# Optimization experiments

Hardware: AMD Instinct MI355X
Metric: run time of the kernel (lower is better)

## Reference

```python
import jax, jax.numpy as jnp
import numpy as np

B, N, C = 8, 1024, 768
H = 12
HD = C // H
R = 16  # LoRA rank
SCALE = HD ** -0.5


def setup_inputs() -> dict:
    key = jax.random.key(0)
    ks = jax.random.split(key, 13)
    s = C ** -0.5
    return {
        "x": jax.random.normal(ks[0], (B, N, C), jnp.float32),
        "Wq": jax.random.normal(ks[1], (C, C), jnp.float32) * s,
        "Wk": jax.random.normal(ks[2], (C, C), jnp.float32) * s,
        "Wv": jax.random.normal(ks[3], (C, C), jnp.float32) * s,
        "Wp": jax.random.normal(ks[4], (C, C), jnp.float32) * s,
        "bp": jax.random.normal(ks[5], (C,), jnp.float32) * 0.02,
        "la_q": jax.random.normal(ks[6], (C, R), jnp.float32) * s,
        "lb_q": jax.random.normal(ks[7], (R, C), jnp.float32) * (R ** -0.5),
        "la_k": jax.random.normal(ks[8], (C, R), jnp.float32) * s,
        "lb_k": jax.random.normal(ks[9], (R, C), jnp.float32) * (R ** -0.5),
        "la_v": jax.random.normal(ks[10], (C, R), jnp.float32) * s,
        "lb_v": jax.random.normal(ks[11], (R, C), jnp.float32) * (R ** -0.5),
        "block_weight": jax.random.uniform(ks[12], (3,), jnp.float32),
    }


def _split_heads(t):
    # [B, N, C] -> [B, H, N, HD]
    return t.reshape(B, N, H, HD).transpose(0, 2, 1, 3)


def reference(x, Wq, Wk, Wv, Wp, bp, la_q, lb_q, la_k, lb_k, la_v, lb_v, block_weight):
    # q/k/v projections (qkv_bias=False) + LoRA adapter injection (msa=[1,1,1])
    q = x @ Wq + block_weight[0] * ((x @ la_q) @ lb_q)
    k = x @ Wk + block_weight[1] * ((x @ la_k) @ lb_k)
    v = x @ Wv + block_weight[2] * ((x @ la_v) @ lb_v)

    qh = _split_heads(q)  # [B,H,N,HD]
    kh = _split_heads(k)
    vh = _split_heads(v)

    # full NxN scores, scale, softmax (attn_drop=0 -> identity)
    attn = jnp.einsum("bhnd,bhmd->bhnm", qh, kh) * SCALE
    attn = jax.nn.softmax(attn, axis=-1)
    out = jnp.einsum("bhnm,bhmd->bhnd", attn, vh)  # [B,H,N,HD]
    out = out.transpose(0, 2, 1, 3).reshape(B, N, C)

    # output projection (proj_drop=0 -> identity)
    return out @ Wp + bp
```

## Files before the change

kernel.cpp:

```cpp
#include <hip/hip_runtime.h>

#define BB 8
#define NN 1024
#define CC 768
#define HH 12
#define HD 64
#define RR 16
#define MM (BB * NN)
#define WSZ (CC * CC)

#define KSC 0.18033688011112042f

typedef short bf16x8 __attribute__((ext_vector_type(8)));
typedef short bf16x4 __attribute__((ext_vector_type(4)));
typedef float f32x4 __attribute__((ext_vector_type(4)));

__device__ __forceinline__ unsigned short f2bf(float f) {
    unsigned u = __builtin_bit_cast(unsigned, f);
    unsigned r = (u + 0x7FFFu + ((u >> 16) & 1u)) >> 16;
    return (unsigned short)r;
}
__device__ __forceinline__ float bf2f(unsigned short s) {
    return __builtin_bit_cast(float, ((unsigned)s) << 16);
}

__global__ __launch_bounds__(256) void prep_w(
    const float* __restrict__ Wq, const float* __restrict__ Wk,
    const float* __restrict__ Wv, const float* __restrict__ Wp,
    const float* __restrict__ la_q, const float* __restrict__ lb_q,
    const float* __restrict__ la_k, const float* __restrict__ lb_k,
    const float* __restrict__ la_v, const float* __restrict__ lb_v,
    const float* __restrict__ bw, short* __restrict__ wt_hi,
    short* __restrict__ wt_lo) {
    __shared__ float laS[64][16];
    __shared__ float lbS[16][64];
    __shared__ float T[64][65];

    const int z = blockIdx.z;
    const int k0 = blockIdx.y * 64, n0 = blockIdx.x * 64;
    const int tid = threadIdx.x;

    const float* W = (z == 0) ? Wq : (z == 1) ? Wk : (z == 2) ? Wv : Wp;
    const float* la = (z == 0) ? la_q : (z == 1) ? la_k : la_v;
    const float* lb = (z == 0) ? lb_q : (z == 1) ? lb_k : lb_v;
    const float bwz = (z < 3) ? bw[z] : 0.f;

    if (z < 3) {
        #pragma unroll
        for (int e = 0; e < 4; ++e) {
            int idx = tid + 256 * e;
            laS[idx >> 4][idx & 15] = la[(size_t)(k0 + (idx >> 4)) * RR + (idx & 15)];
            lbS[idx >> 6][idx & 63] = lb[(size_t)(idx >> 6) * CC + n0 + (idx & 63)];
        }
    }
    __syncthreads();

    #pragma unroll
    for (int e = 0; e < 16; ++e) {
        int idx = tid + 256 * e;
        int row = idx >> 6, col = idx & 63;
        float v = W[(size_t)(k0 + row) * CC + n0 + col];
        if (z < 3) {
            float s = 0.f;
            #pragma unroll
            for (int r = 0; r < 16; ++r) s += laS[row][r] * lbS[r][col];
            v += bwz * s;
        }
        T[row][col] = v;
    }
    __syncthreads();

    short* oh = wt_hi + (size_t)z * WSZ;
    short* ol = wt_lo + (size_t)z * WSZ;
    #pragma unroll
    for (int e = 0; e < 16; ++e) {
        int idx = tid + 256 * e;
        int nrow = idx >> 6, kcol = idx & 63;
        float v = T[kcol][nrow];
        unsigned short hi = f2bf(v);
        unsigned short lo = f2bf(v - bf2f(hi));
        size_t off = (size_t)(n0 + nrow) * CC + k0 + kcol;
        oh[off] = (short)hi;
        ol[off] = (short)lo;
    }
}

__global__ __launch_bounds__(256) void prep_cvt(const float* __restrict__ src,
                                                short* __restrict__ hi,
                                                short* __restrict__ lo, int n4) {
    int i = blockIdx.x * 256 + threadIdx.x;
    const int stride = gridDim.x * 256;
    for (; i < n4; i += stride) {
        f32x4 v = ((const f32x4*)src)[i];
        bf16x4 h, l;
        #pragma unroll
        for (int c = 0; c < 4; ++c) {
            unsigned short hh = f2bf(v[c]);
            h[c] = (short)hh;
            l[c] = (short)f2bf(v[c] - bf2f(hh));
        }
        ((bf16x4*)hi)[i] = h;
        ((bf16x4*)lo)[i] = l;
    }
}

#define LW 40

__device__ __forceinline__ void gemm_core(
    const short* __restrict__ gAh, const short* __restrict__ gAl, int rowA0,
    const short* __restrict__ gBh, const short* __restrict__ gBl, int rowB0,
    short* AsH, short* AsL, short* BsH, short* BsL, f32x4 acc[4][4]) {
    const int tid = threadIdx.x;
    const int lane = tid & 63;
    const int w = tid >> 6;
    const int wm = w >> 1, wn = w & 1;
    const int p = lane & 15, g = lane >> 4;

    const int srow = tid >> 2;
    const int scc = (tid & 3) * 8;

    for (int kt = 0; kt < CC; kt += 32) {
        #pragma unroll
        for (int q = 0; q < 2; ++q) {
            int row = srow + 64 * q;
            size_t ga = (size_t)(rowA0 + row) * CC + kt + scc;
            size_t gb = (size_t)(rowB0 + row) * CC + kt + scc;
            bf16x8 ah = *(const bf16x8*)(gAh + ga);
            bf16x8 al = *(const bf16x8*)(gAl + ga);
            bf16x8 bh = *(const bf16x8*)(gBh + gb);
            bf16x8 bl = *(const bf16x8*)(gBl + gb);
            *(bf16x8*)(AsH + row * LW + scc) = ah;
            *(bf16x8*)(AsL + row * LW + scc) = al;
            *(bf16x8*)(BsH + row * LW + scc) = bh;
            *(bf16x8*)(BsL + row * LW + scc) = bl;
        }
        __syncthreads();

        bf16x8 a_h[4], a_l[4], b_h[4], b_l[4];
        #pragma unroll
        for (int i = 0; i < 4; ++i) {
            int arow = wm * 64 + i * 16 + p;
            int brow = wn * 64 + i * 16 + p;
            a_h[i] = *(const bf16x8*)(AsH + arow * LW + g * 8);
            a_l[i] = *(const bf16x8*)(AsL + arow * LW + g * 8);
            b_h[i] = *(const bf16x8*)(BsH + brow * LW + g * 8);
            b_l[i] = *(const bf16x8*)(BsL + brow * LW + g * 8);
        }
        #pragma unroll
        for (int i = 0; i < 4; ++i) {
            #pragma unroll
            for (int j = 0; j < 4; ++j) {
                acc[i][j] = __builtin_amdgcn_mfma_f32_16x16x32_bf16(
                    a_h[i], b_h[j], acc[i][j], 0, 0, 0);
                acc[i][j] = __builtin_amdgcn_mfma_f32_16x16x32_bf16(
                    a_h[i], b_l[j], acc[i][j], 0, 0, 0);
                acc[i][j] = __builtin_amdgcn_mfma_f32_16x16x32_bf16(
                    a_l[i], b_h[j], acc[i][j], 0, 0, 0);
            }
        }
        __syncthreads();
    }
}

__global__ __launch_bounds__(256, 2) void gemm_qkv(
    const short* __restrict__ xh, const short* __restrict__ xl,
    const short* __restrict__ wth, const short* __restrict__ wtl,
    short* __restrict__ qb, short* __restrict__ kb, short* __restrict__ vtb) {
    __shared__ __align__(16) short AsH[128 * LW], AsL[128 * LW];
    __shared__ __align__(16) short BsH[128 * LW], BsL[128 * LW];

    const int z = blockIdx.z;
    const int m0 = blockIdx.y * 128, c0 = blockIdx.x * 128;
    const short* wzh = wth + (size_t)z * WSZ;
    const short* wzl = wtl + (size_t)z * WSZ;

    f32x4 acc[4][4];
    const f32x4 z4 = {0.f, 0.f, 0.f, 0.f};
    #pragma unroll
    for (int i = 0; i < 4; ++i)
        #pragma unroll
        for (int j = 0; j < 4; ++j) acc[i][j] = z4;

    const int lane = threadIdx.x & 63, w = threadIdx.x >> 6;
    const int wm = w >> 1, wn = w & 1, p = lane & 15, g = lane >> 4;

    if (z < 2) {
        gemm_core(xh, xl, m0, wzh, wzl, c0, AsH, AsL, BsH, BsL, acc);
        short* dst = (z == 0) ? qb : kb;
        #pragma unroll
        for (int i = 0; i < 4; ++i) {
            #pragma unroll
            for (int r = 0; r < 4; ++r) {
                int m = m0 + wm * 64 + i * 16 + 4 * g + r;
                int b = m >> 10, n = m & 1023;
                #pragma unroll
                for (int j = 0; j < 4; ++j) {
                    int c = c0 + wn * 64 + j * 16 + p;
                    int h = c >> 6, d = c & 63;
                    dst[(((size_t)(b * HH + h)) * NN + n) * HD + d] =
                        (short)f2bf(acc[i][j][r]);
                }
            }
        }
    } else {
        gemm_core(wzh, wzl, c0, xh, xl, m0, AsH, AsL, BsH, BsL, acc);
        #pragma unroll
        for (int i = 0; i < 4; ++i) {
            #pragma unroll
            for (int r = 0; r < 4; ++r) {
                int c = c0 + wm * 64 + i * 16 + 4 * g + r;
                int h = c >> 6, d = c & 63;
                #pragma unroll
                for (int j = 0; j < 4; ++j) {
                    int m = m0 + wn * 64 + j * 16 + p;
                    int b = m >> 10, n = m & 1023;
                    vtb[(((size_t)(b * HH + h)) * HD + d) * NN + n] =
                        (short)f2bf(acc[i][j][r]);
                }
            }
        }
    }
}

#define AW 72

__global__ __launch_bounds__(256) void attn(const short* __restrict__ qb,
                                            const short* __restrict__ kb,
                                            const short* __restrict__ vtb,
                                            short* __restrict__ aoh,
                                            short* __restrict__ aol) {
    __shared__ __align__(16) short Qs[64 * AW], Ks[64 * AW], Vts[64 * AW];
    __shared__ __align__(16) short Ps[4][16 * AW];

    const int bh = blockIdx.y, q0 = blockIdx.x * 64;
    const int tid = threadIdx.x, lane = tid & 63, w = tid >> 6;
    const int p = lane & 15, g = lane >> 4;
    const short* qp = qb + (size_t)bh * NN * HD;
    const short* kp = kb + (size_t)bh * NN * HD;
    const short* vp = vtb + (size_t)bh * NN * HD;

    #pragma unroll
    for (int e = 0; e < 2; ++e) {
        int idx = tid + 256 * e;
        int row = idx >> 3, c8 = (idx & 7) * 8;
        *(bf16x8*)(Qs + row * AW + c8) =
            *(const bf16x8*)(qp + (size_t)(q0 + row) * HD + c8);
    }
    __syncthreads();
    bf16x8 bQ[2];
    #pragma unroll
    for (int ks = 0; ks < 2; ++ks)
        bQ[ks] = *(const bf16x8*)(Qs + (w * 16 + p) * AW + g * 8 + 32 * ks);

    float m_run = -1e30f, l_run = 0.f;
    f32x4 oacc[4];
    const f32x4 z4 = {0.f, 0.f, 0.f, 0.f};
    #pragma unroll
    for (int df = 0; df < 4; ++df) oacc[df] = z4;
    short* Pw = &Ps[w][0];

    for (int t = 0; t < NN / 64; ++t) {
        if (t) __syncthreads();
        const int j0 = t * 64;
        #pragma unroll
        for (int e = 0; e < 2; ++e) {
            int idx = tid + 256 * e;
            int row = idx >> 3, c8 = (idx & 7) * 8;
            *(bf16x8*)(Ks + row * AW + c8) =
                *(const bf16x8*)(kp + (size_t)(j0 + row) * HD + c8);
            *(bf16x8*)(Vts + row * AW + c8) =
                *(const bf16x8*)(vp + (size_t)row * NN + j0 + c8);
        }
        __syncthreads();

        f32x4 sacc[4];
        #pragma unroll
        for (int jf = 0; jf < 4; ++jf) sacc[jf] = z4;
        #pragma unroll
        for (int ks = 0; ks < 2; ++ks) {
            #pragma unroll
            for (int jf = 0; jf < 4; ++jf) {
                bf16x8 aK =
                    *(const bf16x8*)(Ks + (jf * 16 + p) * AW + g * 8 + 32 * ks);
                sacc[jf] = __builtin_amdgcn_mfma_f32_16x16x32_bf16(
                    aK, bQ[ks], sacc[jf], 0, 0, 0);
            }
        }

        float tmax = -1e30f;
        #pragma unroll
        for (int jf = 0; jf < 4; ++jf)
            #pragma unroll
            for (int r = 0; r < 4; ++r) tmax = fmaxf(tmax, sacc[jf][r]);
        tmax = fmaxf(tmax, __shfl_xor(tmax, 16));
        tmax = fmaxf(tmax, __shfl_xor(tmax, 32));
        const float mnew = fmaxf(m_run, tmax);
        const float fac = exp2f((m_run - mnew) * KSC);
        m_run = mnew;
        float lsum = 0.f;
        bf16x4 pk[4];
        #pragma unroll
        for (int jf = 0; jf < 4; ++jf) {
            #pragma unroll
            for (int r = 0; r < 4; ++r) {
                float e = exp2f((sacc[jf][r] - mnew) * KSC);
                lsum += e;
                pk[jf][r] = (short)f2bf(e);
            }
        }
        lsum += __shfl_xor(lsum, 16);
        lsum += __shfl_xor(lsum, 32);
        l_run = l_run * fac + lsum;

        #pragma unroll
        for (int jf = 0; jf < 4; ++jf)
            *(bf16x4*)(Pw + p * AW + jf * 16 + 4 * g) = pk[jf];
        asm volatile("s_waitcnt lgkmcnt(0)" ::: "memory");
        __builtin_amdgcn_sched_barrier(0);

        #pragma unroll
        for (int r = 0; r < 4; ++r) {
            float fr = __shfl(fac, 4 * g + r, 16);
            #pragma unroll
            for (int df = 0; df < 4; ++df) oacc[df][r] *= fr;
        }

        #pragma unroll
        for (int ks = 0; ks < 2; ++ks) {
            bf16x8 aP = *(const bf16x8*)(Pw + p * AW + g * 8 + 32 * ks);
            #pragma unroll
            for (int df = 0; df < 4; ++df) {
                bf16x8 bV =
                    *(const bf16x8*)(Vts + (df * 16 + p) * AW + g * 8 + 32 * ks);
                oacc[df] = __builtin_amdgcn_mfma_f32_16x16x32_bf16(
                    aP, bV, oacc[df], 0, 0, 0);
            }
        }
    }

    const float inv = 1.f / l_run;
    const int b = bh / HH, h = bh % HH;
    #pragma unroll
    for (int r = 0; r < 4; ++r) {
        float ir = __shfl(inv, 4 * g + r, 16);
        int n = q0 + w * 16 + 4 * g + r;
        #pragma unroll
        for (int df = 0; df < 4; ++df) {
            float v = oacc[df][r] * ir;
            unsigned short hi = f2bf(v);
            unsigned short lo = f2bf(v - bf2f(hi));
            size_t off = ((size_t)(b * NN + n)) * CC + h * HD + df * 16 + p;
            aoh[off] = (short)hi;
            aol[off] = (short)lo;
        }
    }
}

__global__ __launch_bounds__(256, 2) void gemm_proj(
    const short* __restrict__ aoh, const short* __restrict__ aol,
    const short* __restrict__ wth, const short* __restrict__ wtl,
    const float* __restrict__ bp, float* __restrict__ out) {
    __shared__ __align__(16) short AsH[128 * LW], AsL[128 * LW];
    __shared__ __align__(16) short BsH[128 * LW], BsL[128 * LW];

    const int m0 = blockIdx.y * 128, c0 = blockIdx.x * 128;
    const short* wph = wth + (size_t)3 * WSZ;
    const short* wpl = wtl + (size_t)3 * WSZ;

    f32x4 acc[4][4];
    const f32x4 z4 = {0.f, 0.f, 0.f, 0.f};
    #pragma unroll
    for (int i = 0; i < 4; ++i)
        #pragma unroll
        for (int j = 0; j < 4; ++j) acc[i][j] = z4;

    gemm_core(aoh, aol, m0, wph, wpl, c0, AsH, AsL, BsH, BsL, acc);

    const int lane = threadIdx.x & 63, w = threadIdx.x >> 6;
    const int wm = w >> 1, wn = w & 1, p = lane & 15, g = lane >> 4;

    float bpv[4];
    #pragma unroll
    for (int j = 0; j < 4; ++j) bpv[j] = bp[c0 + wn * 64 + j * 16 + p];

    #pragma unroll
    for (int i = 0; i < 4; ++i) {
        #pragma unroll
        for (int r = 0; r < 4; ++r) {
            int m = m0 + wm * 64 + i * 16 + 4 * g + r;
            #pragma unroll
            for (int j = 0; j < 4; ++j) {
                int c = c0 + wn * 64 + j * 16 + p;
                out[(size_t)m * CC + c] = acc[i][j][r] + bpv[j];
            }
        }
    }
}

extern "C" void kernel_launch(void* const* d_in, const int* in_sizes, int n_in,
                              void* d_out, int out_size, void* d_ws,
                              size_t ws_size, hipStream_t stream) {
    const float* x = (const float*)d_in[0];
    const float* Wq = (const float*)d_in[1];
    const float* Wk = (const float*)d_in[2];
    const float* Wv = (const float*)d_in[3];
    const float* Wp = (const float*)d_in[4];
    const float* bp = (const float*)d_in[5];
    const float* la_q = (const float*)d_in[6];
    const float* lb_q = (const float*)d_in[7];
    const float* la_k = (const float*)d_in[8];
    const float* lb_k = (const float*)d_in[9];
    const float* la_v = (const float*)d_in[10];
    const float* lb_v = (const float*)d_in[11];
    const float* bw = (const float*)d_in[12];
    float* out = (float*)d_out;

    short* ws = (short*)d_ws;
    short* wt_hi = ws;
    short* wt_lo = wt_hi + (size_t)4 * WSZ;
    short* x_hi = wt_lo + (size_t)4 * WSZ;
    short* x_lo = x_hi + (size_t)MM * CC;
    short* qbuf = x_lo + (size_t)MM * CC;
    short* kbuf = qbuf + (size_t)MM * CC;
    short* vtbuf = kbuf + (size_t)MM * CC;
    short* aoh = vtbuf + (size_t)MM * CC;
    short* aol = aoh + (size_t)MM * CC;

    prep_w<<<dim3(CC / 64, CC / 64, 4), 256, 0, stream>>>(
        Wq, Wk, Wv, Wp, la_q, lb_q, la_k, lb_k, la_v, lb_v, bw, wt_hi, wt_lo);
    prep_cvt<<<2048, 256, 0, stream>>>(x, x_hi, x_lo, MM * CC / 4);
    gemm_qkv<<<dim3(CC / 128, MM / 128, 3), 256, 0, stream>>>(
        x_hi, x_lo, wt_hi, wt_lo, qbuf, kbuf, vtbuf);
    attn<<<dim3(NN / 64, BB * HH), 256, 0, stream>>>(qbuf, kbuf, vtbuf, aoh, aol);
    gemm_proj<<<dim3(CC / 128, MM / 128), 256, 0, stream>>>(aoh, aol, wt_hi,
                                                            wt_lo, bp, out);
}
```

Baseline: 331.4 us.

## Double-buffer GEMM and attention tiles with direct global-to-LDS loads and XCD swizzle

Replaces register-staged global loads with global_load_lds into MFMA-fragment-ordered LDS layouts, double-buffered so the next K tile (GEMMs) or K/V tile (attention) loads while the current one computes. Adds block-index swizzling so neighbouring tiles land on the same XCD for L2 reuse. Attention also skips the rescale of the output accumulator when no row max changes, using a wave-wide __any check. LDS use grows (64KB per GEMM block), which may limit occupancy, and correctness relies on the async LDS writes being complete at each barrier.

```diff
diff --git a/kernel.cpp b/kernel.cpp
--- a/kernel.cpp
+++ b/kernel.cpp
@@ -8,6 +8,7 @@
 #define RR 16
 #define MM (BB * NN)
 #define WSZ (CC * CC)
+#define NT (NN / 64)
 
 #define KSC 0.18033688011112042f
 
@@ -22,6 +23,12 @@
 }
 __device__ __forceinline__ float bf2f(unsigned short s) {
     return __builtin_bit_cast(float, ((unsigned)s) << 16);
+}
+
+__device__ __forceinline__ void gload16(const void* g, void* l) {
+    __builtin_amdgcn_global_load_lds(
+        (const __attribute__((address_space(1))) unsigned int*)g,
+        (__attribute__((address_space(3))) unsigned int*)l, 16, 0, 0);
 }
 
 __global__ __launch_bounds__(256) void prep_w(
@@ -104,60 +111,76 @@
     }
 }
 
-#define LW 40
-
-__device__ __forceinline__ void gemm_core(
-    const short* __restrict__ gAh, const short* __restrict__ gAl, int rowA0,
-    const short* __restrict__ gBh, const short* __restrict__ gBl, int rowB0,
-    short* AsH, short* AsL, short* BsH, short* BsL, f32x4 acc[4][4]) {
-    const int tid = threadIdx.x;
-    const int lane = tid & 63;
-    const int w = tid >> 6;
+__device__ __forceinline__ void stage_gemm(const short* __restrict__ gAh,
+                                           const short* __restrict__ gAl,
+                                           const short* __restrict__ gBh,
+                                           const short* __restrict__ gBl,
+                                           int rowA0, int rowB0, int kt,
+                                           short* Lb, int tid) {
+    const int fr = ((tid >> 6) << 4) | (tid & 15);
+    const int kc = ((tid >> 4) & 3) * 8 + kt;
+    const size_t ga0 = (size_t)(rowA0 + fr) * CC + kc;
+    const size_t ga1 = ga0 + (size_t)64 * CC;
+    const size_t gb0 = (size_t)(rowB0 + fr) * CC + kc;
+    const size_t gb1 = gb0 + (size_t)64 * CC;
+    short* d0 = Lb + tid * 8;
+    short* d1 = Lb + (tid + 256) * 8;
+    gload16(gAh + ga0, d0);
+    gload16(gAh + ga1, d1);
+    gload16(gAl + ga0, d0 + 4096);
+    gload16(gAl + ga1, d1 + 4096);
+    gload16(gBh + gb0, d0 + 8192);
+    gload16(gBh + gb1, d1 + 8192);
+    gload16(gBl + gb0, d0 + 12288);
+    gload16(gBl + gb1, d1 + 12288);
+}
+
+__device__ __forceinline__ void gemm_compute(const short* Lb, int wm, int wn,
+                                             int lane, f32x4 acc[4][4]) {
+    const int fb = lane * 8;
+    const short* AH = Lb;
+    const short* AL = Lb + 4096;
+    const short* BH = Lb + 8192;
+    const short* BL = Lb + 12288;
+    bf16x8 ah[4], al[4], bh[4], bl[4];
+    #pragma unroll
+    for (int i = 0; i < 4; ++i) {
+        ah[i] = *(const bf16x8*)(AH + (wm * 4 + i) * 512 + fb);
+        al[i] = *(const bf16x8*)(AL + (wm * 4 + i) * 512 + fb);
+    }
+    #pragma unroll
+    for (int j = 0; j < 4; ++j) {
+        bh[j] = *(const bf16x8*)(BH + (wn * 4 + j) * 512 + fb);
+        bl[j] = *(const bf16x8*)(BL + (wn * 4 + j) * 512 + fb);
+    }
+    #pragma unroll
+    for (int i = 0; i < 4; ++i) {
+        #pragma unroll
+        for (int j = 0; j < 4; ++j) {
+            acc[i][j] = __builtin_amdgcn_mfma_f32_16x16x32_bf16(ah[i], bh[j],
+                                                                acc[i][j], 0, 0, 0);
+            acc[i][j] = __builtin_amdgcn_mfma_f32_16x16x32_bf16(ah[i], bl[j],
+                                                                acc[i][j], 0, 0, 0);
+            acc[i][j] = __builtin_amdgcn_mfma_f32_16x16x32_bf16(al[i], bh[j],
+                                                                acc[i][j], 0, 0, 0);
+        }
+    }
+}
+
+__device__ __forceinline__ void gemm_core(const short* __restrict__ gAh,
+                                          const short* __restrict__ gAl, int rowA0,
+                                          const short* __restrict__ gBh,
+                                          const short* __restrict__ gBl, int rowB0,
+                                          short (*L)[4 * 4096], f32x4 acc[4][4]) {
+    const int tid = threadIdx.x, lane = tid & 63, w = tid >> 6;
     const int wm = w >> 1, wn = w & 1;
-    const int p = lane & 15, g = lane >> 4;
-
-    const int srow = tid >> 2;
-    const int scc = (tid & 3) * 8;
-
-    for (int kt = 0; kt < CC; kt += 32) {
-        #pragma unroll
-        for (int q = 0; q < 2; ++q) {
-            int row = srow + 64 * q;
-            size_t ga = (size_t)(rowA0 + row) * CC + kt + scc;
-            size_t gb = (size_t)(rowB0 + row) * CC + kt + scc;
-            bf16x8 ah = *(const bf16x8*)(gAh + ga);
-            bf16x8 al = *(const bf16x8*)(gAl + ga);
-            bf16x8 bh = *(const bf16x8*)(gBh + gb);
-            bf16x8 bl = *(const bf16x8*)(gBl + gb);
-            *(bf16x8*)(AsH + row * LW + scc) = ah;
-            *(bf16x8*)(AsL + row * LW + scc) = al;
-            *(bf16x8*)(BsH + row * LW + scc) = bh;
-            *(bf16x8*)(BsL + row * LW + scc) = bl;
-        }
-        __syncthreads();
-
-        bf16x8 a_h[4], a_l[4], b_h[4], b_l[4];
-        #pragma unroll
-        for (int i = 0; i < 4; ++i) {
-            int arow = wm * 64 + i * 16 + p;
-            int brow = wn * 64 + i * 16 + p;
-            a_h[i] = *(const bf16x8*)(AsH + arow * LW + g * 8);
-            a_l[i] = *(const bf16x8*)(AsL + arow * LW + g * 8);
-            b_h[i] = *(const bf16x8*)(BsH + brow * LW + g * 8);
-            b_l[i] = *(const bf16x8*)(BsL + brow * LW + g * 8);
-        }
-        #pragma unroll
-        for (int i = 0; i < 4; ++i) {
-            #pragma unroll
-            for (int j = 0; j < 4; ++j) {
-                acc[i][j] = __builtin_amdgcn_mfma_f32_16x16x32_bf16(
-                    a_h[i], b_h[j], acc[i][j], 0, 0, 0);
-                acc[i][j] = __builtin_amdgcn_mfma_f32_16x16x32_bf16(
-                    a_h[i], b_l[j], acc[i][j], 0, 0, 0);
-                acc[i][j] = __builtin_amdgcn_mfma_f32_16x16x32_bf16(
-                    a_l[i], b_h[j], acc[i][j], 0, 0, 0);
-            }
-        }
+    stage_gemm(gAh, gAl, gBh, gBl, rowA0, rowB0, 0, L[0], tid);
+    __syncthreads();
+    for (int ki = 0; ki < 24; ++ki) {
+        if (ki < 23)
+            stage_gemm(gAh, gAl, gBh, gBl, rowA0, rowB0, (ki + 1) * 32,
+                       L[(ki + 1) & 1], tid);
+        gemm_compute(L[ki & 1], wm, wn, lane, acc);
         __syncthreads();
     }
 }
@@ -166,11 +189,15 @@
     const short* __restrict__ xh, const short* __restrict__ xl,
     const short* __restrict__ wth, const short* __restrict__ wtl,
     short* __restrict__ qb, short* __restrict__ kb, short* __restrict__ vtb) {
-    __shared__ __align__(16) short AsH[128 * LW], AsL[128 * LW];
-    __shared__ __align__(16) short BsH[128 * LW], BsL[128 * LW];
-
-    const int z = blockIdx.z;
-    const int m0 = blockIdx.y * 128, c0 = blockIdx.x * 128;
+    __shared__ __align__(16) short L[2][4 * 4096];
+
+    int flat = blockIdx.x + 6 * blockIdx.y + 384 * blockIdx.z;
+    int swz = (flat & 7) * 144 + (flat >> 3);
+    int z = swz / 384;
+    int rem = swz - z * 384;
+    int by = rem / 6, bx = rem - by * 6;
+    const int m0 = by * 128, c0 = bx * 128;
+
     const short* wzh = wth + (size_t)z * WSZ;
     const short* wzl = wtl + (size_t)z * WSZ;
 
@@ -185,7 +212,7 @@
     const int wm = w >> 1, wn = w & 1, p = lane & 15, g = lane >> 4;
 
     if (z < 2) {
-        gemm_core(xh, xl, m0, wzh, wzl, c0, AsH, AsL, BsH, BsL, acc);
+        gemm_core(xh, xl, m0, wzh, wzl, c0, L, acc);
         short* dst = (z == 0) ? qb : kb;
         #pragma unroll
         for (int i = 0; i < 4; ++i) {
@@ -203,7 +230,7 @@
             }
         }
     } else {
-        gemm_core(wzh, wzl, c0, xh, xl, m0, AsH, AsL, BsH, BsL, acc);
+        gemm_core(wzh, wzl, c0, xh, xl, m0, L, acc);
         #pragma unroll
         for (int i = 0; i < 4; ++i) {
             #pragma unroll
@@ -222,56 +249,65 @@
     }
 }
 
-#define AW 72
+__device__ __forceinline__ void stage_kv(const short* __restrict__ kp,
+                                         const short* __restrict__ vp, int j0,
+                                         short* Kd, short* Vd, int tid) {
+    const int pp = tid & 15;
+    const int kc = ((tid >> 4) & 3) * 8 + ((tid >> 6) & 1) * 32;
+    const int r0 = tid >> 7;
+    gload16(kp + (size_t)(j0 + r0 * 16 + pp) * HD + kc, Kd + tid * 8);
+    gload16(kp + (size_t)(j0 + (r0 + 2) * 16 + pp) * HD + kc, Kd + (tid + 256) * 8);
+    gload16(vp + (size_t)(r0 * 16 + pp) * NN + j0 + kc, Vd + tid * 8);
+    gload16(vp + (size_t)((r0 + 2) * 16 + pp) * NN + j0 + kc, Vd + (tid + 256) * 8);
+}
 
 __global__ __launch_bounds__(256) void attn(const short* __restrict__ qb,
                                             const short* __restrict__ kb,
                                             const short* __restrict__ vtb,
                                             short* __restrict__ aoh,
                                             short* __restrict__ aol) {
-    __shared__ __align__(16) short Qs[64 * AW], Ks[64 * AW], Vts[64 * AW];
-    __shared__ __align__(16) short Ps[4][16 * AW];
-
-    const int bh = blockIdx.y, q0 = blockIdx.x * 64;
+    __shared__ __align__(16) short Qs[4096];
+    __shared__ __align__(16) short Kb[2][4096];
+    __shared__ __align__(16) short Vb[2][4096];
+    __shared__ __align__(16) short Ps[4096];
+
+    int flat = blockIdx.x + 16 * blockIdx.y;
+    int swz = (flat & 7) * 192 + (flat >> 3);
+    const int q0 = (swz & 15) * 64;
+    const int bh = swz >> 4;
+
     const int tid = threadIdx.x, lane = tid & 63, w = tid >> 6;
     const int p = lane & 15, g = lane >> 4;
     const short* qp = qb + (size_t)bh * NN * HD;
     const short* kp = kb + (size_t)bh * NN * HD;
     const short* vp = vtb + (size_t)bh * NN * HD;
 
-    #pragma unroll
-    for (int e = 0; e < 2; ++e) {
-        int idx = tid + 256 * e;
-        int row = idx >> 3, c8 = (idx & 7) * 8;
-        *(bf16x8*)(Qs + row * AW + c8) =
-            *(const bf16x8*)(qp + (size_t)(q0 + row) * HD + c8);
-    }
+    {
+        const int kc = ((tid >> 4) & 3) * 8 + ((tid >> 6) & 1) * 32;
+        const int r0 = tid >> 7;
+        gload16(qp + (size_t)(q0 + r0 * 16 + p) * HD + kc, Qs + tid * 8);
+        gload16(qp + (size_t)(q0 + (r0 + 2) * 16 + p) * HD + kc,
+                Qs + (tid + 256) * 8);
+    }
+    stage_kv(kp, vp, 0, Kb[0], Vb[0], tid);
     __syncthreads();
+
     bf16x8 bQ[2];
-    #pragma unroll
-    for (int ks = 0; ks < 2; ++ks)
-        bQ[ks] = *(const bf16x8*)(Qs + (w * 16 + p) * AW + g * 8 + 32 * ks);
+    bQ[0] = *(const bf16x8*)(Qs + (w * 2 + 0) * 512 + lane * 8);
+    bQ[1] = *(const bf16x8*)(Qs + (w * 2 + 1) * 512 + lane * 8);
 
     float m_run = -1e30f, l_run = 0.f;
     f32x4 oacc[4];
     const f32x4 z4 = {0.f, 0.f, 0.f, 0.f};
     #pragma unroll
     for (int df = 0; df < 4; ++df) oacc[df] = z4;
-    short* Pw = &Ps[w][0];
-
-    for (int t = 0; t < NN / 64; ++t) {
-        if (t) __syncthreads();
-        const int j0 = t * 64;
-        #pragma unroll
-        for (int e = 0; e < 2; ++e) {
-            int idx = tid + 256 * e;
-            int row = idx >> 3, c8 = (idx & 7) * 8;
-            *(bf16x8*)(Ks + row * AW + c8) =
-                *(const bf16x8*)(kp + (size_t)(j0 + row) * HD + c8);
-            *(bf16x8*)(Vts + row * AW + c8) =
-                *(const bf16x8*)(vp + (size_t)row * NN + j0 + c8);
-        }
-        __syncthreads();
+    short* Pw = Ps + w * 1024;
+
+    for (int t = 0; t < NT; ++t) {
+        if (t < NT - 1)
+            stage_kv(kp, vp, (t + 1) * 64, Kb[(t + 1) & 1], Vb[(t + 1) & 1], tid);
+        const short* Kc = Kb[t & 1];
+        const short* Vc = Vb[t & 1];
 
         f32x4 sacc[4];
         #pragma unroll
@@ -281,7 +317,7 @@
             #pragma unroll
             for (int jf = 0; jf < 4; ++jf) {
                 bf16x8 aK =
-                    *(const bf16x8*)(Ks + (jf * 16 + p) * AW + g * 8 + 32 * ks);
+                    *(const bf16x8*)(Kc + jf * 1024 + ks * 512 + lane * 8);
                 sacc[jf] = __builtin_amdgcn_mfma_f32_16x16x32_bf16(
                     aK, bQ[ks], sacc[jf], 0, 0, 0);
             }
@@ -294,48 +330,53 @@
             for (int r = 0; r < 4; ++r) tmax = fmaxf(tmax, sacc[jf][r]);
         tmax = fmaxf(tmax, __shfl_xor(tmax, 16));
         tmax = fmaxf(tmax, __shfl_xor(tmax, 32));
-        const float mnew = fmaxf(m_run, tmax);
-        const float fac = exp2f((m_run - mnew) * KSC);
-        m_run = mnew;
+        if (__any(tmax > m_run)) {
+            const float mnew = fmaxf(m_run, tmax);
+            const float fac = exp2f((m_run - mnew) * KSC);
+            m_run = mnew;
+            l_run *= fac;
+            #pragma unroll
+            for (int r = 0; r < 4; ++r) {
+                float fr = __shfl(fac, 4 * g + r, 16);
+                #pragma unroll
+                for (int df = 0; df < 4; ++df) oacc[df][r] *= fr;
+            }
+        }
         float lsum = 0.f;
         bf16x4 pk[4];
         #pragma unroll
         for (int jf = 0; jf < 4; ++jf) {
             #pragma unroll
             for (int r = 0; r < 4; ++r) {
-                float e = exp2f((sacc[jf][r] - mnew) * KSC);
+                float e = exp2f((sacc[jf][r] - m_run) * KSC);
                 lsum += e;
                 pk[jf][r] = (short)f2bf(e);
             }
         }
         lsum += __shfl_xor(lsum, 16);
         lsum += __shfl_xor(lsum, 32);
-        l_run = l_run * fac + lsum;
+        l_run += lsum;
 
         #pragma unroll
         for (int jf = 0; jf < 4; ++jf)
-            *(bf16x4*)(Pw + p * AW + jf * 16 + 4 * g) = pk[jf];
+            *(bf16x4*)(Pw + (jf >> 1) * 512 +
+                       (((jf & 1) * 2 + (g >> 1)) * 16 + p) * 8 + (g & 1) * 4) =
+                pk[jf];
         asm volatile("s_waitcnt lgkmcnt(0)" ::: "memory");
         __builtin_amdgcn_sched_barrier(0);
 
         #pragma unroll
-        for (int r = 0; r < 4; ++r) {
-            float fr = __shfl(fac, 4 * g + r, 16);
-            #pragma unroll
-            for (int df = 0; df < 4; ++df) oacc[df][r] *= fr;
-        }
-
-        #pragma unroll
         for (int ks = 0; ks < 2; ++ks) {
-            bf16x8 aP = *(const bf16x8*)(Pw + p * AW + g * 8 + 32 * ks);
+            bf16x8 aP = *(const bf16x8*)(Pw + ks * 512 + lane * 8);
             #pragma unroll
             for (int df = 0; df < 4; ++df) {
                 bf16x8 bV =
-                    *(const bf16x8*)(Vts + (df * 16 + p) * AW + g * 8 + 32 * ks);
+                    *(const bf16x8*)(Vc + df * 1024 + ks * 512 + lane * 8);
                 oacc[df] = __builtin_amdgcn_mfma_f32_16x16x32_bf16(
                     aP, bV, oacc[df], 0, 0, 0);
             }
         }
+        __syncthreads();
     }
 
     const float inv = 1.f / l_run;
@@ -360,10 +401,13 @@
     const short* __restrict__ aoh, const short* __restrict__ aol,
     const short* __restrict__ wth, const short* __restrict__ wtl,
     const float* __restrict__ bp, float* __restrict__ out) {
-    __shared__ __align__(16) short AsH[128 * LW], AsL[128 * LW];
-    __shared__ __align__(16) short BsH[128 * LW], BsL[128 * LW];
-
-    const int m0 = blockIdx.y * 128, c0 = blockIdx.x * 128;
+    __shared__ __align__(16) short L[2][4 * 4096];
+
+    int flat = blockIdx.x + 6 * blockIdx.y;
+    int swz = (flat & 7) * 48 + (flat >> 3);
+    int by = swz / 6, bx = swz - by * 6;
+    const int m0 = by * 128, c0 = bx * 128;
+
     const short* wph = wth + (size_t)3 * WSZ;
     const short* wpl = wtl + (size_t)3 * WSZ;
 
@@ -374,7 +418,7 @@
         #pragma unroll
         for (int j = 0; j < 4; ++j) acc[i][j] = z4;
 
-    gemm_core(aoh, aol, m0, wph, wpl, c0, AsH, AsL, BsH, BsL, acc);
+    gemm_core(aoh, aol, m0, wph, wpl, c0, L, acc);
 
     const int lane = threadIdx.x & 63, w = threadIdx.x >> 6;
     const int wm = w >> 1, wn = w & 1, p = lane & 15, g = lane >> 4;
```

Result: slower. 353.2 us (+6.6%).
